# Optimization experiments

Measured on AMD Instinct MI355X. Metric: run time of the kernel, lower is better.

The kernel has to match this reference:

```python
import jax, jax.numpy as jnp
import numpy as np
from jax import lax

E, DIM, INTER, TOPK, NT = 32, 2048, 1408, 4, 4096
UP = 2 * INTER          # gated activation: interleaved gate/up columns
BLK = 128               # FP8 block-quant tile size
ALPHA, LIMIT, OFFSET = 1.702, 7.0, 1.0  # quick_geglu constants


def setup_inputs() -> dict:
    key = jax.random.key(0)
    ks = jax.random.split(key, 8)
    x = jax.random.normal(ks[0], (NT, DIM), jnp.float32)
    token_mask = jax.random.bernoulli(ks[1], 0.95, (NT,))
    weights = jax.random.uniform(ks[2], (NT, TOPK), jnp.float32)
    indices = jax.random.randint(ks[3], (NT, TOPK), 0, E)
    # frozen FP8 expert weights + block-wise inverse scales (buffers)
    gate_up_w8 = (jax.random.normal(ks[4], (E, DIM, UP), jnp.float32) * 0.05).astype(jnp.float8_e4m3fn)
    down_w8 = (jax.random.normal(ks[5], (E, INTER, DIM), jnp.float32) * 0.05).astype(jnp.float8_e4m3fn)
    gate_up_scale = jax.random.uniform(ks[6], (E, DIM // BLK, UP // BLK), jnp.float32, 0.5, 1.5)
    down_scale = jax.random.uniform(ks[7], (E, INTER // BLK, DIM // BLK), jnp.float32, 0.5, 1.5)
    return dict(x=x, token_mask=token_mask, weights=weights, indices=indices,
                gate_up_w8=gate_up_w8, down_w8=down_w8,
                gate_up_scale=gate_up_scale, down_scale=down_scale)


def _dequant(w8, sinv):
    # block-wise FP8 dequant: w[e, r, c] * sinv[e, r//128, c//128]
    e, r, c = w8.shape
    w = w8.astype(jnp.float32).reshape(e, r // BLK, BLK, c // BLK, BLK)
    return (w * sinv[:, :, None, :, None]).reshape(e, r, c)


def reference(x, token_mask, weights, indices, gate_up_w8, down_w8, gate_up_scale, down_scale):
    nt, topk = indices.shape
    dim = x.shape[1]
    # mask invalid (token_mask=False or out-of-range expert) routing entries
    valid = token_mask[:, None] & (indices >= 0) & (indices < E)
    fvalid = valid.reshape(-1)
    eid = jnp.where(fvalid, indices.reshape(-1), E)  # invalid -> E, sorts last
    tok = jnp.repeat(jnp.arange(nt), topk)
    probs = jnp.where(fvalid, weights.astype(jnp.float32).reshape(-1), 0.0)
    # stable sort by expert id (matches argsort(stable=True) in source)
    order = jnp.argsort(eid, stable=True)
    s_eid, s_tok, s_prob = eid[order], tok[order], probs[order]
    # invalid rows are clamped into the last expert's group; their prob is 0
    # and they scatter to a dummy slot, so they contribute nothing.
    gs = jnp.bincount(jnp.minimum(s_eid, E - 1), length=E).astype(jnp.int32)
    w_gu = _dequant(gate_up_w8, gate_up_scale)   # [E, dim, 2*inter]
    w_d = _dequant(down_w8, down_scale)          # [E, inter, dim]
    h = x[s_tok]                                  # [T, dim] permuted tokens
    o1 = lax.ragged_dot(h, w_gu, gs)              # grouped GEMM 1: [T, 2*inter]
    gate = jnp.minimum(o1[..., ::2], LIMIT)       # interleaved gate/up split
    up = jnp.clip(o1[..., 1::2], -LIMIT, LIMIT)
    inter = gate * jax.nn.sigmoid(ALPHA * gate) * (up + OFFSET) * s_prob[:, None]
    o2 = lax.ragged_dot(inter, w_d, gs)           # grouped GEMM 2: [T, dim]
    dst = jnp.where(s_eid < E, s_tok, nt)         # dummy slot nt for invalid
    out = jnp.zeros((nt + 1, dim), jnp.float32).at[dst].add(o2)
    return out[:nt].astype(x.dtype)
```

## Files before the change

kernel.cpp:

```cpp
#include <hip/hip_runtime.h>
#include <hip/hip_bf16.h>

#define E_ 32
#define DIM_ 2048
#define INTER_ 1408
#define UP_ 2816
#define NT_ 4096
#define NE_ 16384
#define MAXT 96

typedef __attribute__((ext_vector_type(8))) short bf16x8;
typedef __attribute__((ext_vector_type(4))) float f32x4;
typedef unsigned int uint32;
typedef unsigned long long u64t;

struct Meta {
  int gs[E_];
  int offs[E_ + 1];
  int Ttot;
  int ntiles;
  int tile_e[MAXT];
  int tile_r0[MAXT];
};

__device__ __forceinline__ unsigned short bf16_of(float f) {
  union { __hip_bfloat16 b; unsigned short u; } cv;
  cv.b = __float2bfloat16(f);
  return cv.u;
}

__device__ __forceinline__ bool mask_ok(const void* m, int mode, int tok) {
  if (mode) return ((const uint32*)m)[tok] != 0u;
  return ((const unsigned char*)m)[tok] != 0;
}

__global__ __launch_bounds__(256) void k_route(
    const void* __restrict__ tmask, const float* __restrict__ wts,
    const int* __restrict__ idx, Meta* __restrict__ meta,
    int* __restrict__ s_tok, float* __restrict__ s_prob, int* __restrict__ inv) {
  __shared__ unsigned short tc[E_][257];
  __shared__ int offs_s[E_ + 1];
  __shared__ int tot[E_];
  __shared__ int mmode;
  const int t = threadIdx.x;
  if (t == 0) {
    const uint32* w = (const uint32*)tmask;
    bool word_mode = true;
    for (int i = 0; i < 64; ++i) {
      uint32 v = w[i];
      if (!(v <= 1u || v == 0x3F800000u)) { word_mode = false; break; }
    }
    mmode = word_mode ? 1 : 0;
  }
#pragma unroll
  for (int e = 0; e < E_; ++e) tc[e][t] = 0;
  __syncthreads();
  const int base = t * 64;
  for (int i = 0; i < 64; ++i) {
    int ent = base + i;
    int e = idx[ent];
    bool v = mask_ok(tmask, mmode, ent >> 2) && (e >= 0) && (e < E_);
    if (v) tc[e][t] += 1;
  }
  __syncthreads();
  if (t < E_) {
    int run = 0;
    for (int j = 0; j < 256; ++j) {
      int c = tc[t][j]; tc[t][j] = (unsigned short)run; run += c;
    }
    tot[t] = run;
  }
  __syncthreads();
  if (t == 0) {
    int acc = 0, nt = 0;
    for (int e = 0; e < E_; ++e) {
      offs_s[e] = acc;
      meta->offs[e] = acc;
      meta->gs[e] = tot[e];
      for (int r0 = 0; r0 < tot[e]; r0 += 256) {
        meta->tile_e[nt] = e; meta->tile_r0[nt] = r0; ++nt;
      }
      acc += tot[e];
    }
    offs_s[E_] = acc;
    meta->offs[E_] = acc;
    meta->Ttot = acc;
    meta->ntiles = nt;
  }
  __syncthreads();
  for (int i = 0; i < 64; ++i) {
    int ent = base + i;
    int e = idx[ent];
    bool v = mask_ok(tmask, mmode, ent >> 2) && (e >= 0) && (e < E_);
    if (v) {
      int r = tc[e][t]++;
      int pos = offs_s[e] + r;
      s_tok[pos] = ent >> 2;
      s_prob[pos] = wts[ent];
      inv[ent] = pos;
    } else {
      inv[ent] = -1;
    }
  }
}

__global__ __launch_bounds__(256) void k_xcast(const float* __restrict__ x,
                                               unsigned short* __restrict__ xb) {
  const size_t i = ((size_t)blockIdx.x * 256 + threadIdx.x) * 8;
  f32x4 a = *(const f32x4*)(x + i);
  f32x4 b = *(const f32x4*)(x + i + 4);
  uint4 o;
  o.x = (uint32)bf16_of(a.x) | ((uint32)bf16_of(a.y) << 16);
  o.y = (uint32)bf16_of(a.z) | ((uint32)bf16_of(a.w) << 16);
  o.z = (uint32)bf16_of(b.x) | ((uint32)bf16_of(b.y) << 16);
  o.w = (uint32)bf16_of(b.z) | ((uint32)bf16_of(b.w) << 16);
  *(uint4*)(xb + i) = o;
}

template <int KTOT, int NTOT, bool GEGLU, bool GATHER>
__global__ __launch_bounds__(512) void k_gemm(
    const float* __restrict__ Wf, const float* __restrict__ scale,
    const unsigned short* __restrict__ Asrc, const Meta* __restrict__ meta,
    const int* __restrict__ s_tok, const float* __restrict__ s_prob,
    unsigned short* __restrict__ o_bf16, float* __restrict__ o_f32, int staged) {
  constexpr int NX = NTOT / 128;
  constexpr int NKS = KTOT / 64;
  const int NBact = NX * meta->ntiles;
  const int bid = blockIdx.x;
  if (bid >= NBact) return;
  const int q = NBact >> 3, r = NBact & 7;
  const int x = bid & 7, pos = bid >> 3;
  const int wk = ((x < r) ? x * (q + 1) : r * (q + 1) + (x - r) * q) + pos;
  const int tile = wk / NX;
  const int n0 = (wk % NX) * 128;
  const int e = meta->tile_e[tile];
  const int row0 = meta->tile_r0[tile];
  const int off = meta->offs[e];
  const int gsz = meta->gs[e];

  __shared__ unsigned short As[256 * 64];
  __shared__ unsigned short Bs[128 * 64];

  const int tid = threadIdx.x;
  const int lane = tid & 63;
  const int wid = tid >> 6;
  const int wm = wid >> 1;
  const int wn = wid & 1;

  const char* aSrc[4];
  {
    const int rr = lane >> 3, cc = lane & 7;
#pragma unroll
    for (int i = 0; i < 4; ++i) {
      const int grow = row0 + wid * 32 + i * 8 + rr;
      int slot;
      if (GATHER) slot = (grow < gsz) ? s_tok[off + grow] : 0;
      else slot = off + grow;
      const int key = rr ^ ((wid * 4 + i) & 7);
      aSrc[i] = (const char*)Asrc + (size_t)slot * (KTOT * 2) + ((cc ^ key) << 4);
    }
  }

  const int kq = tid >> 5;
  const int kc = kq >> 1;
  const int half = kq & 1;
  const int n4 = (tid & 31) * 4;

  const float* Bbase = Wf + (size_t)e * KTOT * NTOT + n0;
  const float* sbase = scale + (size_t)e * (KTOT / 128) * (NTOT / 128) + (n0 >> 7);

  f32x4 acc[4][4] = {};
  f32x4 v[4];

#define LOAD_B(KS)                                                             \
  {                                                                            \
    const float* Bk = Bbase + (size_t)((KS) * 64 + kq * 4) * NTOT + n4;        \
    _Pragma("unroll") for (int i = 0; i < 4; ++i)                              \
      v[i] = *(const f32x4*)(Bk + (size_t)i * NTOT);                           \
  }

#define ISSUE_A(KS)                                                            \
  {                                                                            \
    _Pragma("unroll") for (int i = 0; i < 4; ++i) {                            \
      __builtin_amdgcn_global_load_lds(                                        \
          (const __attribute__((address_space(1))) uint32*)(aSrc[i] + (size_t)(KS) * 128), \
          (__attribute__((address_space(3))) uint32*)(&As[(wid * 32 + i * 8) * 64]), \
          16, 0, 0);                                                           \
    }                                                                          \
  }

#define WRITE_B(KS)                                                            \
  {                                                                            \
    const float bscl = sbase[((KS) >> 1) * (NTOT / 128)];                      \
    _Pragma("unroll") for (int j = 0; j < 4; ++j) {                            \
      const int n = n4 + j;                                                    \
      const int key = (n & 7) ^ ((n >> 3) & 7);                                \
      uint32 lo = (uint32)bf16_of(v[0][j] * bscl) | ((uint32)bf16_of(v[1][j] * bscl) << 16); \
      uint32 hi = (uint32)bf16_of(v[2][j] * bscl) | ((uint32)bf16_of(v[3][j] * bscl) << 16); \
      *(u64t*)&Bs[n * 64 + ((kc ^ key) << 3) + half * 4] = (u64t)lo | ((u64t)hi << 32); \
    }                                                                          \
  }

  LOAD_B(0);

  for (int ks = 0; ks < NKS; ++ks) {
    __syncthreads();
    ISSUE_A(ks);
    WRITE_B(ks);
    __syncthreads();
    if (ks + 1 < NKS) LOAD_B(ks + 1);
#pragma unroll
    for (int sub = 0; sub < 2; ++sub) {
      const int c0 = sub * 4 + (lane >> 4);
      bf16x8 a[4], b[4];
#pragma unroll
      for (int fI = 0; fI < 4; ++fI) {
        const int ra = wm * 64 + fI * 16 + (lane & 15);
        const int ka = c0 ^ (ra & 7) ^ ((ra >> 3) & 7);
        a[fI] = *(const bf16x8*)&As[ra * 64 + (ka << 3)];
        const int rb = wn * 64 + fI * 16 + (lane & 15);
        const int kb = c0 ^ (rb & 7) ^ ((rb >> 3) & 7);
        b[fI] = *(const bf16x8*)&Bs[rb * 64 + (kb << 3)];
      }
#pragma unroll
      for (int fm = 0; fm < 4; ++fm)
#pragma unroll
        for (int fn = 0; fn < 4; ++fn)
          acc[fm][fn] = __builtin_amdgcn_mfma_f32_16x16x32_bf16(a[fm], b[fn], acc[fm][fn], 0, 0, 0);
    }
  }
#undef LOAD_B
#undef ISSUE_A
#undef WRITE_B

  const int nbase = n0 + wn * 64;
#pragma unroll
  for (int fm = 0; fm < 4; ++fm) {
#pragma unroll
    for (int r2 = 0; r2 < 4; ++r2) {
      const int rl = row0 + wm * 64 + fm * 16 + (lane >> 4) * 4 + r2;
      const bool ok = rl < gsz;
      const int slot = off + rl;
      if constexpr (GEGLU) {
        const float p = ok ? s_prob[slot] : 0.f;
#pragma unroll
        for (int fn = 0; fn < 4; ++fn) {
          float vv = acc[fm][fn][r2];
          float vp = __shfl_xor(vv, 1, 64);
          float g = (lane & 1) ? vp : vv;
          float u = (lane & 1) ? vv : vp;
          g = fminf(g, 7.f);
          u = fminf(fmaxf(u, -7.f), 7.f);
          const float sig = 1.f / (1.f + __expf(-1.702f * g));
          const float val = g * sig * (u + 1.f) * p;
          if (ok && !(lane & 1)) {
            const int c = (nbase + fn * 16 + (lane & 15)) >> 1;
            o_bf16[(size_t)slot * INTER_ + c] = bf16_of(val);
          }
        }
      } else {
        if (staged) {
          float* orow = o_f32 + (size_t)slot * DIM_;
          if (ok) {
#pragma unroll
            for (int fn = 0; fn < 4; ++fn)
              orow[nbase + fn * 16 + (lane & 15)] = acc[fm][fn][r2];
          }
        } else {
          if (ok) {
            float* orow = o_f32 + (size_t)s_tok[slot] * DIM_;
#pragma unroll
            for (int fn = 0; fn < 4; ++fn)
              atomicAdd(&orow[nbase + fn * 16 + (lane & 15)], acc[fm][fn][r2]);
          }
        }
      }
    }
  }
}

__global__ __launch_bounds__(256) void k_reduce(const float* __restrict__ o2s,
                                                const int* __restrict__ inv,
                                                float* __restrict__ out) {
  const int t = blockIdx.x;
  const int c = threadIdx.x * 8;
  f32x4 s0 = {0.f, 0.f, 0.f, 0.f}, s1 = {0.f, 0.f, 0.f, 0.f};
#pragma unroll
  for (int j = 0; j < 4; ++j) {
    const int sl = inv[t * 4 + j];
    if (sl >= 0) {
      const float* r = o2s + (size_t)sl * DIM_ + c;
      f32x4 a = *(const f32x4*)r;
      f32x4 b = *(const f32x4*)(r + 4);
      s0 += a; s1 += b;
    }
  }
  float* o = out + (size_t)t * DIM_ + c;
  *(f32x4*)o = s0;
  *(f32x4*)(o + 4) = s1;
}

extern "C" void kernel_launch(void* const* d_in, const int* in_sizes, int n_in,
                              void* d_out, int out_size, void* d_ws, size_t ws_size,
                              hipStream_t stream) {
  const float* x = (const float*)d_in[0];
  const void* tmask = d_in[1];
  const float* wts = (const float*)d_in[2];
  const int* idx = (const int*)d_in[3];
  const float* gup_w = (const float*)d_in[4];
  const float* dn_w = (const float*)d_in[5];
  const float* gup_sc = (const float*)d_in[6];
  const float* dn_sc = (const float*)d_in[7];
  float* out = (float*)d_out;
  char* ws = (char*)d_ws;

  const size_t xb_off = 262144;
  const size_t inter_off = xb_off + (size_t)NT_ * DIM_ * 2;
  const size_t o2s_off = inter_off + (size_t)(NE_ + 256) * INTER_ * 2;
  const size_t need = o2s_off;
  const size_t need2 = o2s_off + (size_t)(NE_ + 256) * DIM_ * 4;
  if (ws_size < need) return;
  const int staged = (ws_size >= need2) ? 1 : 0;

  Meta* meta = (Meta*)(ws);
  int* s_tok = (int*)(ws + 4096);
  float* s_prob = (float*)(ws + 4096 + NE_ * 4);
  int* inv = (int*)(ws + 4096 + 2 * NE_ * 4);
  unsigned short* xb = (unsigned short*)(ws + xb_off);
  unsigned short* inter = (unsigned short*)(ws + inter_off);
  float* o2s = (float*)(ws + o2s_off);

  if (!staged)
    (void)hipMemsetAsync(d_out, 0, (size_t)out_size * sizeof(float), stream);
  hipLaunchKernelGGL(k_route, dim3(1), dim3(256), 0, stream, tmask, wts, idx, meta, s_tok, s_prob, inv);
  hipLaunchKernelGGL(k_xcast, dim3(NT_ * DIM_ / 2048), dim3(256), 0, stream, x, xb);
  hipLaunchKernelGGL((k_gemm<DIM_, UP_, true, true>), dim3((UP_ / 128) * MAXT), dim3(512), 0,
                     stream, gup_w, gup_sc, xb, meta, s_tok, s_prob, inter, (float*)nullptr, 0);
  hipLaunchKernelGGL((k_gemm<INTER_, DIM_, false, false>), dim3((DIM_ / 128) * MAXT), dim3(512), 0,
                     stream, dn_w, dn_sc, inter, meta, s_tok, s_prob, (unsigned short*)nullptr,
                     staged ? o2s : out, staged);
  if (staged)
    hipLaunchKernelGGL(k_reduce, dim3(NT_), dim3(256), 0, stream, o2s, inv, out);
}
```

Measured before the change: 823.2 us.

## Double-buffer B register prefetch with manual waitcnt pipelining in grouped GEMM

Restructures the GEMM main loop into a two-stage software pipeline. It alternates two register buffers for the fp32 weight loads, so loads two k-steps ahead stay in flight, and uses explicit s_waitcnt and s_barrier with sched_barrier fences instead of __syncthreads. It also adds a min-blocks hint of 4 to launch_bounds, which caps register use. This aims to hide global load latency for the weight stream, but adds register pressure and relies on correct vmcnt counting for the LDS DMA and global loads.

Result: slower. 1.821 ms (+121.2%).

```diff
diff --git a/kernel.cpp b/kernel.cpp
--- a/kernel.cpp
+++ b/kernel.cpp
@@ -118,7 +118,7 @@
 }
 
 template <int KTOT, int NTOT, bool GEGLU, bool GATHER>
-__global__ __launch_bounds__(512) void k_gemm(
+__global__ __launch_bounds__(512, 4) void k_gemm(
     const float* __restrict__ Wf, const float* __restrict__ scale,
     const unsigned short* __restrict__ Asrc, const Meta* __restrict__ meta,
     const int* __restrict__ s_tok, const float* __restrict__ s_prob,
@@ -170,13 +170,13 @@
   const float* sbase = scale + (size_t)e * (KTOT / 128) * (NTOT / 128) + (n0 >> 7);
 
   f32x4 acc[4][4] = {};
-  f32x4 v[4];
-
-#define LOAD_B(KS)                                                             \
+  f32x4 v0[4], v1[4];
+
+#define LOAD_B(KS, V)                                                          \
   {                                                                            \
     const float* Bk = Bbase + (size_t)((KS) * 64 + kq * 4) * NTOT + n4;        \
     _Pragma("unroll") for (int i = 0; i < 4; ++i)                              \
-      v[i] = *(const f32x4*)(Bk + (size_t)i * NTOT);                           \
+      V[i] = *(const f32x4*)(Bk + (size_t)i * NTOT);                           \
   }
 
 #define ISSUE_A(KS)                                                            \
@@ -189,49 +189,78 @@
     }                                                                          \
   }
 
-#define WRITE_B(KS)                                                            \
+#define WRITE_B(KS, V)                                                         \
   {                                                                            \
     const float bscl = sbase[((KS) >> 1) * (NTOT / 128)];                      \
     _Pragma("unroll") for (int j = 0; j < 4; ++j) {                            \
       const int n = n4 + j;                                                    \
       const int key = (n & 7) ^ ((n >> 3) & 7);                                \
-      uint32 lo = (uint32)bf16_of(v[0][j] * bscl) | ((uint32)bf16_of(v[1][j] * bscl) << 16); \
-      uint32 hi = (uint32)bf16_of(v[2][j] * bscl) | ((uint32)bf16_of(v[3][j] * bscl) << 16); \
+      uint32 lo = (uint32)bf16_of(V[0][j] * bscl) | ((uint32)bf16_of(V[1][j] * bscl) << 16); \
+      uint32 hi = (uint32)bf16_of(V[2][j] * bscl) | ((uint32)bf16_of(V[3][j] * bscl) << 16); \
       *(u64t*)&Bs[n * 64 + ((kc ^ key) << 3) + half * 4] = (u64t)lo | ((u64t)hi << 32); \
     }                                                                          \
   }
 
-  LOAD_B(0);
-
-  for (int ks = 0; ks < NKS; ++ks) {
-    __syncthreads();
-    ISSUE_A(ks);
-    WRITE_B(ks);
-    __syncthreads();
-    if (ks + 1 < NKS) LOAD_B(ks + 1);
-#pragma unroll
-    for (int sub = 0; sub < 2; ++sub) {
-      const int c0 = sub * 4 + (lane >> 4);
-      bf16x8 a[4], b[4];
-#pragma unroll
-      for (int fI = 0; fI < 4; ++fI) {
-        const int ra = wm * 64 + fI * 16 + (lane & 15);
-        const int ka = c0 ^ (ra & 7) ^ ((ra >> 3) & 7);
-        a[fI] = *(const bf16x8*)&As[ra * 64 + (ka << 3)];
-        const int rb = wn * 64 + fI * 16 + (lane & 15);
-        const int kb = c0 ^ (rb & 7) ^ ((rb >> 3) & 7);
-        b[fI] = *(const bf16x8*)&Bs[rb * 64 + (kb << 3)];
-      }
-#pragma unroll
-      for (int fm = 0; fm < 4; ++fm)
-#pragma unroll
-        for (int fn = 0; fn < 4; ++fn)
-          acc[fm][fn] = __builtin_amdgcn_mfma_f32_16x16x32_bf16(a[fm], b[fn], acc[fm][fn], 0, 0, 0);
+#define MFMA_STEP()                                                            \
+  {                                                                            \
+    _Pragma("unroll") for (int sub = 0; sub < 2; ++sub) {                      \
+      const int c0 = sub * 4 + (lane >> 4);                                    \
+      bf16x8 a[4], b[4];                                                       \
+      _Pragma("unroll") for (int fI = 0; fI < 4; ++fI) {                       \
+        const int ra = wm * 64 + fI * 16 + (lane & 15);                        \
+        const int ka = c0 ^ (ra & 7) ^ ((ra >> 3) & 7);                        \
+        a[fI] = *(const bf16x8*)&As[ra * 64 + (ka << 3)];                      \
+        const int rb = wn * 64 + fI * 16 + (lane & 15);                        \
+        const int kb = c0 ^ (rb & 7) ^ ((rb >> 3) & 7);                        \
+        b[fI] = *(const bf16x8*)&Bs[rb * 64 + (kb << 3)];                      \
+      }                                                                        \
+      _Pragma("unroll") for (int fm = 0; fm < 4; ++fm)                         \
+        _Pragma("unroll") for (int fn = 0; fn < 4; ++fn)                       \
+          acc[fm][fn] = __builtin_amdgcn_mfma_f32_16x16x32_bf16(a[fm], b[fn], acc[fm][fn], 0, 0, 0); \
+    }                                                                          \
+  }
+
+  LOAD_B(0, v0);
+  LOAD_B(1, v1);
+  ISSUE_A(0);
+  __builtin_amdgcn_sched_barrier(0);
+  WRITE_B(0, v0);
+  LOAD_B(2, v0);
+  __builtin_amdgcn_sched_barrier(0);
+  asm volatile("s_waitcnt lgkmcnt(0)" ::: "memory");
+  asm volatile("s_waitcnt vmcnt(8)" ::: "memory");
+  __builtin_amdgcn_s_barrier();
+
+  for (int ks = 0; ks < NKS; ks += 2) {
+    MFMA_STEP();
+    __builtin_amdgcn_s_barrier();
+    ISSUE_A(ks + 1);
+    __builtin_amdgcn_sched_barrier(0);
+    WRITE_B(ks + 1, v1);
+    if (ks + 3 < NKS) LOAD_B(ks + 3, v1);
+    __builtin_amdgcn_sched_barrier(0);
+    asm volatile("s_waitcnt lgkmcnt(0)" ::: "memory");
+    if (ks + 3 < NKS) asm volatile("s_waitcnt vmcnt(8)" ::: "memory");
+    else              asm volatile("s_waitcnt vmcnt(0)" ::: "memory");
+    __builtin_amdgcn_s_barrier();
+    MFMA_STEP();
+    if (ks + 2 < NKS) {
+      __builtin_amdgcn_s_barrier();
+      ISSUE_A(ks + 2);
+      __builtin_amdgcn_sched_barrier(0);
+      WRITE_B(ks + 2, v0);
+      if (ks + 4 < NKS) LOAD_B(ks + 4, v0);
+      __builtin_amdgcn_sched_barrier(0);
+      asm volatile("s_waitcnt lgkmcnt(0)" ::: "memory");
+      if (ks + 4 < NKS) asm volatile("s_waitcnt vmcnt(8)" ::: "memory");
+      else              asm volatile("s_waitcnt vmcnt(0)" ::: "memory");
+      __builtin_amdgcn_s_barrier();
     }
   }
 #undef LOAD_B
 #undef ISSUE_A
 #undef WRITE_B
+#undef MFMA_STEP
 
   const int nbase = n0 + wn * 64;
 #pragma unroll
```

## Shrink grouped GEMM M-tile to 128 rows with 256-thread blocks

Applied to the files above, without the earlier changes.

Changes the routing tile size from 256 to 128 rows per expert, halves the A shared-memory tile, and runs the GEMM kernels with 256 threads per block instead of 512. B loading is remapped so each thread loads 8 columns instead of 4, with a new swizzle key. The aim is to cut padding waste in partially filled expert tiles and raise occupancy and block count. The cost is reloading and re-dequantizing B weights for twice as many M-tiles. The unseen compute section must still match the new wave layout.

Result: slower. 901.7 us (+9.5%).

```diff
diff --git a/kernel.cpp b/kernel.cpp
--- a/kernel.cpp
+++ b/kernel.cpp
@@ -7,7 +7,7 @@
 #define UP_ 2816
 #define NT_ 4096
 #define NE_ 16384
-#define MAXT 96
+#define MAXTILES 160
 
 typedef __attribute__((ext_vector_type(8))) short bf16x8;
 typedef __attribute__((ext_vector_type(4))) float f32x4;
@@ -19,8 +19,8 @@
   int offs[E_ + 1];
   int Ttot;
   int ntiles;
-  int tile_e[MAXT];
-  int tile_r0[MAXT];
+  int tile_e[MAXTILES];
+  int tile_r0[MAXTILES];
 };
 
 __device__ __forceinline__ unsigned short bf16_of(float f) {
@@ -77,7 +77,7 @@
       offs_s[e] = acc;
       meta->offs[e] = acc;
       meta->gs[e] = tot[e];
-      for (int r0 = 0; r0 < tot[e]; r0 += 256) {
+      for (int r0 = 0; r0 < tot[e]; r0 += 128) {
         meta->tile_e[nt] = e; meta->tile_r0[nt] = r0; ++nt;
       }
       acc += tot[e];
@@ -118,7 +118,7 @@
 }
 
 template <int KTOT, int NTOT, bool GEGLU, bool GATHER>
-__global__ __launch_bounds__(512) void k_gemm(
+__global__ __launch_bounds__(256) void k_gemm(
     const float* __restrict__ Wf, const float* __restrict__ scale,
     const unsigned short* __restrict__ Asrc, const Meta* __restrict__ meta,
     const int* __restrict__ s_tok, const float* __restrict__ s_prob,
@@ -138,7 +138,7 @@
   const int off = meta->offs[e];
   const int gsz = meta->gs[e];
 
-  __shared__ unsigned short As[256 * 64];
+  __shared__ unsigned short As[128 * 64];
   __shared__ unsigned short Bs[128 * 64];
 
   const int tid = threadIdx.x;
@@ -161,22 +161,27 @@
     }
   }
 
-  const int kq = tid >> 5;
-  const int kc = kq >> 1;
-  const int half = kq & 1;
-  const int n4 = (tid & 31) * 4;
+  const int rg = tid >> 4;
+  const int kc = rg >> 1;
+  const int half = rg & 1;
+  const int a16 = tid & 15;
+  const int nb = a16 * 8;
 
   const float* Bbase = Wf + (size_t)e * KTOT * NTOT + n0;
   const float* sbase = scale + (size_t)e * (KTOT / 128) * (NTOT / 128) + (n0 >> 7);
 
   f32x4 acc[4][4] = {};
-  f32x4 v[4];
+  float v[4][8];
 
 #define LOAD_B(KS)                                                             \
   {                                                                            \
-    const float* Bk = Bbase + (size_t)((KS) * 64 + kq * 4) * NTOT + n4;        \
-    _Pragma("unroll") for (int i = 0; i < 4; ++i)                              \
-      v[i] = *(const f32x4*)(Bk + (size_t)i * NTOT);                           \
+    const float* Bk = Bbase + (size_t)((KS) * 64 + rg * 4) * NTOT + nb;        \
+    _Pragma("unroll") for (int i = 0; i < 4; ++i) {                            \
+      f32x4 a = *(const f32x4*)(Bk + (size_t)i * NTOT);                        \
+      f32x4 b = *(const f32x4*)(Bk + (size_t)i * NTOT + 4);                    \
+      v[i][0] = a.x; v[i][1] = a.y; v[i][2] = a.z; v[i][3] = a.w;              \
+      v[i][4] = b.x; v[i][5] = b.y; v[i][6] = b.z; v[i][7] = b.w;              \
+    }                                                                          \
   }
 
 #define ISSUE_A(KS)                                                            \
@@ -192,9 +197,9 @@
 #define WRITE_B(KS)                                                            \
   {                                                                            \
     const float bscl = sbase[((KS) >> 1) * (NTOT / 128)];                      \
-    _Pragma("unroll") for (int j = 0; j < 4; ++j) {                            \
-      const int n = n4 + j;                                                    \
-      const int key = (n & 7) ^ ((n >> 3) & 7);                                \
+    _Pragma("unroll") for (int j = 0; j < 8; ++j) {                            \
+      const int n = nb + j;                                                    \
+      const int key = j ^ (a16 & 7);                     \
       uint32 lo = (uint32)bf16_of(v[0][j] * bscl) | ((uint32)bf16_of(v[1][j] * bscl) << 16); \
       uint32 hi = (uint32)bf16_of(v[2][j] * bscl) | ((uint32)bf16_of(v[3][j] * bscl) << 16); \
       *(u64t*)&Bs[n * 64 + ((kc ^ key) << 3) + half * 4] = (u64t)lo | ((u64t)hi << 32); \
@@ -334,9 +339,9 @@
     (void)hipMemsetAsync(d_out, 0, (size_t)out_size * sizeof(float), stream);
   hipLaunchKernelGGL(k_route, dim3(1), dim3(256), 0, stream, tmask, wts, idx, meta, s_tok, s_prob, inv);
   hipLaunchKernelGGL(k_xcast, dim3(NT_ * DIM_ / 2048), dim3(256), 0, stream, x, xb);
-  hipLaunchKernelGGL((k_gemm<DIM_, UP_, true, true>), dim3((UP_ / 128) * MAXT), dim3(512), 0,
+  hipLaunchKernelGGL((k_gemm<DIM_, UP_, true, true>), dim3((UP_ / 128) * MAXTILES), dim3(256), 0,
                      stream, gup_w, gup_sc, xb, meta, s_tok, s_prob, inter, (float*)nullptr, 0);
-  hipLaunchKernelGGL((k_gemm<INTER_, DIM_, false, false>), dim3((DIM_ / 128) * MAXT), dim3(512), 0,
+  hipLaunchKernelGGL((k_gemm<INTER_, DIM_, false, false>), dim3((DIM_ / 128) * MAXTILES), dim3(256), 0,
                      stream, dn_w, dn_sc, inter, meta, s_tok, s_prob, (unsigned short*)nullptr,
                      staged ? o2s : out, staged);
   if (staged)
```
